# Kernel optimization log

Hardware: AMD Instinct MI355X
Metric: run time of the kernel (lower is better)

Reference implementation:

```python
import jax, jax.numpy as jnp
import numpy as np

B, L, D = 2, 2048, 1024
H = 16
HD = D // H  # 64


def setup_inputs() -> dict:
    key = jax.random.key(0)
    ks = jax.random.split(key, 7)
    s = 0.02
    return {
        "x": jax.random.normal(ks[0], (B, L, D), dtype=jnp.float32),
        "Wq": jax.random.normal(ks[1], (D, D), dtype=jnp.float32) * s,
        "bq": jnp.zeros((D,), dtype=jnp.float32),
        "Wkv": jax.random.normal(ks[2], (D, 2 * D), dtype=jnp.float32) * s,
        "bkv": jnp.zeros((2 * D,), dtype=jnp.float32),
        "Wo": jax.random.normal(ks[3], (D, D), dtype=jnp.float32) * s,
        "bo": jnp.zeros((D,), dtype=jnp.float32),
    }


def reference(x, Wq, bq, Wkv, bkv, Wo, bo):
    # q/kv projections (self-attention: key/value come from x)
    q = x @ Wq + bq                      # [B, L, D]
    kv = x @ Wkv + bkv                   # [B, L, 2D]
    k, v = jnp.split(kv, 2, axis=-1)     # each [B, L, D]
    # split heads: 'b l (h c) -> b h l c' (rope_embed_fraction=0 -> RoPE is identity)
    def heads(t):
        return t.reshape(B, L, H, HD).transpose(0, 2, 1, 3)
    qh, kh, vh = heads(q), heads(k), heads(v)   # [B, H, L, HD]
    scale = 1.0 / jnp.sqrt(jnp.asarray(HD, dtype=x.dtype))
    scores = jnp.einsum('bhqc,bhkc->bhqk', qh, kh) * scale  # [B, H, L, L]
    attn = jax.nn.softmax(scores, axis=-1)
    y = jnp.einsum('bhqk,bhkc->bhqc', attn, vh)             # [B, H, L, HD]
    # merge heads: 'b h l c -> b l (h c)'
    y = y.transpose(0, 2, 1, 3).reshape(B, L, D)
    return (y @ Wo + bo).reshape(x.shape)
```

## Files before the change

### kernel.cpp

```cpp
#include <hip/hip_runtime.h>

#define B_  2
#define L_  2048
#define D_  1024
#define H_  16
#define HD_ 64

typedef __attribute__((ext_vector_type(8))) short bf16x8;
typedef __attribute__((ext_vector_type(4))) float f32x4;

#define MFMA16(a, b, c) __builtin_amdgcn_mfma_f32_16x16x32_bf16(a, b, c, 0, 0, 0)

__device__ __forceinline__ unsigned short f2bf(float f) {
    union { float f; unsigned u; } v; v.f = f;
    unsigned r = v.u + 0x7FFFu + ((v.u >> 16) & 1u);
    return (unsigned short)(r >> 16);
}

__global__ __launch_bounds__(256) void prep_all(
    const float* __restrict__ x,
    const float* __restrict__ Wq, const float* __restrict__ Wkv,
    const float* __restrict__ Wo,
    unsigned short* __restrict__ xb,
    unsigned short* __restrict__ Wqt, unsigned short* __restrict__ Wkvt,
    unsigned short* __restrict__ Wot)
{
    const int z = blockIdx.z;
    if (z == 4) {
        const int bidl = blockIdx.y * 32 + blockIdx.x;
        const int n4 = B_ * L_ * D_ / 4;
        for (int i = bidl * 256 + threadIdx.x; i < n4; i += 1024 * 256) {
            float4 v = *(const float4*)(x + (size_t)i * 4);
            ushort4 u;
            u.x = f2bf(v.x); u.y = f2bf(v.y); u.z = f2bf(v.z); u.w = f2bf(v.w);
            *(ushort4*)(xb + (size_t)i * 4) = u;
        }
        return;
    }
    __shared__ float t[32][33];
    const float* W;  unsigned short* Wt;  int N, nc;
    if (z == 0)      { W = Wq;  Wt = Wqt;  N = 1024; nc = 0; }
    else if (z == 1) { W = Wo;  Wt = Wot;  N = 1024; nc = 0; }
    else             { W = Wkv; Wt = Wkvt; N = 2048; nc = (z - 2) * 1024; }
    const int tx = threadIdx.x & 31, ty = threadIdx.x >> 5;
    const int n0 = nc + blockIdx.x * 32, k0 = blockIdx.y * 32;
    #pragma unroll
    for (int r = 0; r < 4; ++r)
        t[ty + r * 8][tx] = W[(size_t)(k0 + ty + r * 8) * N + n0 + tx];
    __syncthreads();
    #pragma unroll
    for (int r = 0; r < 4; ++r)
        Wt[(size_t)(n0 + ty + r * 8) * 1024 + k0 + tx] = f2bf(t[tx][ty + r * 8]);
}

__global__ __launch_bounds__(512, 1) void gemm_qkv8(
    const unsigned short* __restrict__ A,
    const unsigned short* __restrict__ Bt,
    const float* __restrict__ bq, const float* __restrict__ bkv,
    unsigned short* __restrict__ Qb, unsigned short* __restrict__ Kb,
    unsigned short* __restrict__ Vtg, float qscl)
{
    const int KDIM = 1024, NT = 16;
    __shared__ __align__(16) unsigned short lds[65536];

    const int tid = threadIdx.x;
    const int w = tid >> 6, l = tid & 63, g = l >> 4, ln = l & 15;
    const int wm = (w >> 2) & 1, wn = w & 3;

    const int lin = blockIdx.x;
    const int wg = (lin & 7) * 24 + (lin >> 3);
    const int by = wg / 12, bx = wg % 12;
    const int m0 = by * 256, n0 = bx * 256;

    const int sr8 = w * 8 + (l >> 3);
    const int sc  = (l & 7) ^ ((l >> 3) & 7);
    const unsigned short* Asrc = A  + (size_t)m0 * KDIM + sc * 8;
    const unsigned short* Bsrc = Bt + (size_t)n0 * KDIM + sc * 8;

#define SLOT_A(d, h) (lds + ((d) * 2 + (h)) * 8192)
#define SLOT_B(d, h) (lds + 32768 + ((d) * 2 + (h)) * 8192)

#define STG(slotp, srcp, hh, kt_) do {                                        \
    _Pragma("unroll")                                                         \
    for (int r_ = 0; r_ < 2; ++r_) {                                          \
        const int row_ = (hh) * 128 + r_ * 64 + sr8;                          \
        __builtin_amdgcn_global_load_lds(                                     \
            (const __attribute__((address_space(1))) void*)                   \
                ((srcp) + (size_t)row_ * KDIM + (kt_) * 64),                  \
            (__attribute__((address_space(3))) void*)                         \
                ((slotp) + r_ * 4096 + w * 512 + l * 8),                      \
            16, 0, 0);                                                        \
    }                                                                         \
} while (0)

    f32x4 acc[8][4];
    #pragma unroll
    for (int i = 0; i < 8; ++i)
        #pragma unroll
        for (int j = 0; j < 4; ++j) acc[i][j] = (f32x4){0.f, 0.f, 0.f, 0.f};

    bf16x8 aR[4][2], bB0[2][2], bB1[2][2];

    STG(SLOT_A(0, 0), Asrc, 0, 0);
    STG(SLOT_B(0, 1), Bsrc, 1, 0);
    STG(SLOT_A(0, 1), Asrc, 1, 0);
    STG(SLOT_B(0, 0), Bsrc, 0, 0);
    STG(SLOT_A(1, 0), Asrc, 0, 1);
    STG(SLOT_B(1, 1), Bsrc, 1, 1);

    #pragma unroll 1
    for (int kt = 0; kt < NT; ++kt) {
        const int cur = kt & 1, nxt = cur ^ 1;
        asm volatile("s_waitcnt vmcnt(4)" ::: "memory");
        __builtin_amdgcn_s_barrier();

        #pragma unroll
        for (int mi = 0; mi < 4; ++mi)
            #pragma unroll
            for (int kc = 0; kc < 2; ++kc) {
                const int rho = wm * 64 + mi * 16 + ln, c = kc * 4 + g;
                aR[mi][kc] = *(const bf16x8*)
                    (SLOT_A(cur, 0) + rho * 64 + ((c ^ (rho & 7)) * 8));
            }
        #pragma unroll
        for (int ni = 0; ni < 2; ++ni)
            #pragma unroll
            for (int kc = 0; kc < 2; ++kc) {
                const int rho = wn * 32 + ni * 16 + ln, c = kc * 4 + g;
                bB0[ni][kc] = *(const bf16x8*)
                    (SLOT_B(cur, 0) + rho * 64 + ((c ^ (rho & 7)) * 8));
            }
        if (kt + 1 < NT) STG(SLOT_A(nxt, 1), Asrc, 1, kt + 1);
        __builtin_amdgcn_s_barrier();
        asm volatile("s_waitcnt lgkmcnt(0)" ::: "memory");
        __builtin_amdgcn_s_setprio(1);
        #pragma unroll
        for (int mi = 0; mi < 4; ++mi)
            #pragma unroll
            for (int ni = 0; ni < 2; ++ni) {
                acc[mi][ni] = MFMA16(aR[mi][0], bB0[ni][0], acc[mi][ni]);
                acc[mi][ni] = MFMA16(aR[mi][1], bB0[ni][1], acc[mi][ni]);
            }
        __builtin_amdgcn_s_setprio(0);
        __builtin_amdgcn_s_barrier();

        #pragma unroll
        for (int ni = 0; ni < 2; ++ni)
            #pragma unroll
            for (int kc = 0; kc < 2; ++kc) {
                const int rho = wn * 32 + ni * 16 + ln, c = kc * 4 + g;
                bB1[ni][kc] = *(const bf16x8*)
                    (SLOT_B(cur, 1) + rho * 64 + ((c ^ (rho & 7)) * 8));
            }
        if (kt + 1 < NT) STG(SLOT_B(nxt, 0), Bsrc, 0, kt + 1);
        __builtin_amdgcn_s_barrier();
        asm volatile("s_waitcnt lgkmcnt(0)" ::: "memory");
        __builtin_amdgcn_s_setprio(1);
        #pragma unroll
        for (int mi = 0; mi < 4; ++mi)
            #pragma unroll
            for (int ni = 0; ni < 2; ++ni) {
                acc[mi][2 + ni] = MFMA16(aR[mi][0], bB1[ni][0], acc[mi][2 + ni]);
                acc[mi][2 + ni] = MFMA16(aR[mi][1], bB1[ni][1], acc[mi][2 + ni]);
            }
        __builtin_amdgcn_s_setprio(0);
        __builtin_amdgcn_s_barrier();

        #pragma unroll
        for (int mi = 0; mi < 4; ++mi)
            #pragma unroll
            for (int kc = 0; kc < 2; ++kc) {
                const int rho = wm * 64 + mi * 16 + ln, c = kc * 4 + g;
                aR[mi][kc] = *(const bf16x8*)
                    (SLOT_A(cur, 1) + rho * 64 + ((c ^ (rho & 7)) * 8));
            }
        if (kt + 2 < NT) STG(SLOT_A(cur, 0), Asrc, 0, kt + 2);
        __builtin_amdgcn_s_barrier();
        asm volatile("s_waitcnt lgkmcnt(0)" ::: "memory");
        __builtin_amdgcn_s_setprio(1);
        #pragma unroll
        for (int mi = 0; mi < 4; ++mi)
            #pragma unroll
            for (int ni = 0; ni < 2; ++ni) {
                acc[4 + mi][2 + ni] = MFMA16(aR[mi][0], bB1[ni][0], acc[4 + mi][2 + ni]);
                acc[4 + mi][2 + ni] = MFMA16(aR[mi][1], bB1[ni][1], acc[4 + mi][2 + ni]);
            }
        __builtin_amdgcn_s_setprio(0);
        __builtin_amdgcn_s_barrier();

        if (kt + 2 < NT) STG(SLOT_B(cur, 1), Bsrc, 1, kt + 2);
        __builtin_amdgcn_s_barrier();
        __builtin_amdgcn_s_setprio(1);
        #pragma unroll
        for (int mi = 0; mi < 4; ++mi)
            #pragma unroll
            for (int ni = 0; ni < 2; ++ni) {
                acc[4 + mi][ni] = MFMA16(aR[mi][0], bB0[ni][0], acc[4 + mi][ni]);
                acc[4 + mi][ni] = MFMA16(aR[mi][1], bB0[ni][1], acc[4 + mi][ni]);
            }
        __builtin_amdgcn_s_setprio(0);
        __builtin_amdgcn_s_barrier();
    }
#undef STG
#undef SLOT_A
#undef SLOT_B

    const int region = n0 >> 10;
    if (region == 2) {
        #pragma unroll
        for (int nh = 0; nh < 2; ++nh)
            #pragma unroll
            for (int ni = 0; ni < 2; ++ni) {
                const int d = n0 - 2048 + nh * 128 + wn * 32 + ni * 16 + ln;
                const float bv = bkv[1024 + d];
                #pragma unroll
                for (int mh = 0; mh < 2; ++mh)
                    #pragma unroll
                    for (int mi = 0; mi < 4; ++mi) {
                        const int tok = m0 + mh * 128 + wm * 64 + mi * 16 + g * 4;
                        const int bb = tok >> 11, t4 = tok & 2047;
                        const f32x4 av = acc[mh * 4 + mi][nh * 2 + ni];
                        ushort4 p4;
                        p4.x = f2bf(av[0] + bv); p4.y = f2bf(av[1] + bv);
                        p4.z = f2bf(av[2] + bv); p4.w = f2bf(av[3] + bv);
                        *(ushort4*)(Vtg + ((size_t)bb * 1024 + d) * 2048 + t4) = p4;
                    }
            }
    } else {
        const int isQ = (region == 0);
        const float osc = isQ ? qscl : 1.f;
        #pragma unroll
        for (int nh = 0; nh < 2; ++nh)
            #pragma unroll
            for (int ni = 0; ni < 2; ++ni) {
                const int col = n0 + nh * 128 + wn * 32 + ni * 16 + ln;
                const float bv = isQ ? bq[col] : bkv[col - 1024];
                const int ck = isQ ? col : col - 1024;
                #pragma unroll
                for (int mh = 0; mh < 2; ++mh)
                    #pragma unroll
                    for (int mi = 0; mi < 4; ++mi) {
                        const int row = m0 + mh * 128 + wm * 64 + mi * 16 + g * 4;
                        const f32x4 av = acc[mh * 4 + mi][nh * 2 + ni];
                        #pragma unroll
                        for (int r = 0; r < 4; ++r) {
                            const float vout = (av[r] + bv) * osc;
                            if (isQ)
                                Qb[(size_t)(row + r) * 1024 + ck] = f2bf(vout);
                            else
                                Kb[(size_t)(row + r) * 1024 + ck] = f2bf(vout);
                        }
                    }
            }
    }
}

__global__ __launch_bounds__(256) void gemm_bt2(
    const unsigned short* __restrict__ A,
    const unsigned short* __restrict__ Bt,
    const float* __restrict__ bias,
    float* __restrict__ Cout)
{
    const int N = 1024, K = 1024;
    __shared__ __align__(16) unsigned short As[128 * 64];
    __shared__ __align__(16) unsigned short Bs[64 * 64];
    const int tid = threadIdx.x;
    const int w = tid >> 6, l = tid & 63, g = l >> 4, ln = l & 15;
    const int wm = w >> 1, wn = w & 1;
    const int dd = blockIdx.x;
    const int bid = (dd & 7) * 64 + (dd >> 3);
    const int m0 = (bid >> 4) * 128, n0 = (bid & 15) * 64;

    const int sr8 = w * 8 + (l >> 3);
    const int sc  = (l & 7) ^ ((l >> 3) & 7);
    const unsigned short* Asrc = A  + (size_t)m0 * K + sc * 8;
    const unsigned short* Bsrc = Bt + (size_t)n0 * K + sc * 8;

    f32x4 acc[4][2];
    #pragma unroll
    for (int i = 0; i < 4; ++i)
        #pragma unroll
        for (int j = 0; j < 2; ++j) acc[i][j] = (f32x4){0.f, 0.f, 0.f, 0.f};

    for (int k0 = 0; k0 < K; k0 += 64) {
        #pragma unroll
        for (int r_ = 0; r_ < 4; ++r_)
            __builtin_amdgcn_global_load_lds(
                (const __attribute__((address_space(1))) void*)
                    (Asrc + (size_t)(r_ * 32 + sr8) * K + k0),
                (__attribute__((address_space(3))) void*)
                    (As + r_ * 2048 + w * 512 + l * 8),
                16, 0, 0);
        #pragma unroll
        for (int r_ = 0; r_ < 2; ++r_)
            __builtin_amdgcn_global_load_lds(
                (const __attribute__((address_space(1))) void*)
                    (Bsrc + (size_t)(r_ * 32 + sr8) * K + k0),
                (__attribute__((address_space(3))) void*)
                    (Bs + r_ * 2048 + w * 512 + l * 8),
                16, 0, 0);
        __syncthreads();
        bf16x8 af[4][2], bfr[2][2];
        #pragma unroll
        for (int mi = 0; mi < 4; ++mi)
            #pragma unroll
            for (int kc = 0; kc < 2; ++kc) {
                const int rho = wm * 64 + mi * 16 + ln, c = kc * 4 + g;
                af[mi][kc] = *(const bf16x8*)
                    (As + rho * 64 + ((c ^ (rho & 7)) * 8));
            }
        #pragma unroll
        for (int ni = 0; ni < 2; ++ni)
            #pragma unroll
            for (int kc = 0; kc < 2; ++kc) {
                const int rho = wn * 32 + ni * 16 + ln, c = kc * 4 + g;
                bfr[ni][kc] = *(const bf16x8*)
                    (Bs + rho * 64 + ((c ^ (rho & 7)) * 8));
            }
        __builtin_amdgcn_s_setprio(1);
        #pragma unroll
        for (int mi = 0; mi < 4; ++mi)
            #pragma unroll
            for (int ni = 0; ni < 2; ++ni) {
                acc[mi][ni] = MFMA16(af[mi][0], bfr[ni][0], acc[mi][ni]);
                acc[mi][ni] = MFMA16(af[mi][1], bfr[ni][1], acc[mi][ni]);
            }
        __builtin_amdgcn_s_setprio(0);
        __syncthreads();
    }

    #pragma unroll
    for (int n = 0; n < 2; ++n) {
        const int col = n0 + wn * 32 + n * 16 + ln;
        const float bv = bias[col];
        #pragma unroll
        for (int m = 0; m < 4; ++m) {
            const int row = m0 + wm * 64 + m * 16 + g * 4;
            #pragma unroll
            for (int r = 0; r < 4; ++r)
                Cout[(size_t)(row + r) * N + col] = acc[m][n][r] + bv;
        }
    }
}

__global__ __launch_bounds__(256, 2) void attn_mfma(
    const unsigned short* __restrict__ Qb,
    const unsigned short* __restrict__ Kb,
    const unsigned short* __restrict__ Vtg,
    unsigned short* __restrict__ Yb)
{
    __shared__ __align__(16) unsigned short Ks[2][64 * 64];
    __shared__ __align__(16) unsigned short Vs[2][64 * 64];
    __shared__ __align__(16) unsigned short Pl[4][2][32 * 64];

    const int tid = threadIdx.x;
    const int w = tid >> 6, l = tid & 63, g = l >> 4, ln = l & 15;
    const int dd = blockIdx.x;
    const int bid = (dd & 7) * 64 + (dd >> 3);
    const int qc = bid & 15, h = (bid >> 4) & 15, b = bid >> 8;
    const int qrow = b * L_ + qc * 128 + w * 32;

    const int sub = l >> 3;
    const int scc = (l & 7) ^ sub;
    const unsigned short* ksrc = Kb  + (size_t)(b * L_) * 1024 + h * HD_ + scc * 8;
    const unsigned short* vsrc = Vtg + (size_t)(b * D_ + h * HD_) * 2048 + scc * 8;

#define STAGE(jj, bb) do {                                                    \
    _Pragma("unroll")                                                         \
    for (int i_ = 0; i_ < 2; ++i_) {                                          \
        const int rowK = w * 16 + i_ * 8 + sub;                               \
        __builtin_amdgcn_global_load_lds(                                     \
            (const __attribute__((address_space(1))) void*)                   \
                (ksrc + (size_t)((jj) * 64 + rowK) * 1024),                   \
            (__attribute__((address_space(3))) void*)                         \
                (&Ks[bb][w * 1024 + i_ * 512]), 16, 0, 0);                    \
        __builtin_amdgcn_global_load_lds(                                     \
            (const __attribute__((address_space(1))) void*)                   \
                (vsrc + (size_t)rowK * 2048 + (jj) * 64),                     \
            (__attribute__((address_space(3))) void*)                         \
                (&Vs[bb][w * 1024 + i_ * 512]), 16, 0, 0);                    \
    }                                                                         \
} while (0)

    bf16x8 qa[2][2];
    #pragma unroll
    for (int qt = 0; qt < 2; ++qt)
        #pragma unroll
        for (int c = 0; c < 2; ++c)
            qa[qt][c] = *(const bf16x8*)
                (Qb + (size_t)(qrow + qt * 16 + ln) * D_ + h * HD_ + c * 32 + g * 8);

    f32x4 o[2][4], lacc[2];
    #pragma unroll
    for (int qt = 0; qt < 2; ++qt) {
        #pragma unroll
        for (int dt = 0; dt < 4; ++dt) o[qt][dt] = (f32x4){0.f, 0.f, 0.f, 0.f};
        lacc[qt] = (f32x4){0.f, 0.f, 0.f, 0.f};
    }
    const short one_s = (short)0x3F80;
    const bf16x8 ones = {one_s, one_s, one_s, one_s, one_s, one_s, one_s, one_s};

    unsigned short* Pw = &Pl[w][0][0];
    const int swzl = (ln & 7) << 3;
    const int swp  = (ln & 7) << 1;

    bf16x8 vbA[4][2], vbB[4][2];

#define S_CORE(BUF, PWS, VARR) do {                                           \
    const unsigned short* Kc = &Ks[BUF][0];                                   \
    const unsigned short* Vc = &Vs[BUF][0];                                   \
    bf16x8 kb[4][2];                                                          \
    _Pragma("unroll")                                                         \
    for (int kt = 0; kt < 4; ++kt)                                            \
        _Pragma("unroll")                                                     \
        for (int c = 0; c < 2; ++c)                                           \
            kb[kt][c] = *(const bf16x8*)                                      \
                (Kc + (kt * 16 + ln) * 64 + ((c * 32 + g * 8) ^ swzl));       \
    f32x4 s[2][4];                                                            \
    const f32x4 z = (f32x4){0.f, 0.f, 0.f, 0.f};                              \
    __builtin_amdgcn_s_setprio(1);                                            \
    _Pragma("unroll")                                                         \
    for (int qt = 0; qt < 2; ++qt)                                            \
        _Pragma("unroll")                                                     \
        for (int kt = 0; kt < 4; ++kt) {                                      \
            f32x4 t0 = MFMA16(kb[kt][0], qa[qt][0], z);                       \
            s[qt][kt] = MFMA16(kb[kt][1], qa[qt][1], t0);                     \
        }                                                                     \
    __builtin_amdgcn_s_setprio(0);                                            \
    _Pragma("unroll")                                                         \
    for (int dt = 0; dt < 4; ++dt)                                            \
        _Pragma("unroll")                                                     \
        for (int c2 = 0; c2 < 2; ++c2)                                        \
            VARR[dt][c2] = *(const bf16x8*)                                   \
                (Vc + (dt * 16 + ln) * 64 + ((c2 * 32 + g * 8) ^ swzl));      \
    _Pragma("unroll")                                                         \
    for (int qt = 0; qt < 2; ++qt) {                                          \
        const int prow = (qt * 16 + ln) * 64;                                 \
        _Pragma("unroll")                                                     \
        for (int kt = 0; kt < 4; ++kt) {                                      \
            union { float f; unsigned u; } c0, c1, c2u, c3;                   \
            c0.f = __builtin_exp2f(s[qt][kt][0]);                             \
            c1.f = __builtin_exp2f(s[qt][kt][1]);                             \
            c2u.f = __builtin_exp2f(s[qt][kt][2]);                            \
            c3.f = __builtin_exp2f(s[qt][kt][3]);                             \
            uint2 pk;                                                         \
            pk.x = __builtin_amdgcn_perm(c1.u, c0.u, 0x07060302u);            \
            pk.y = __builtin_amdgcn_perm(c3.u, c2u.u, 0x07060302u);           \
            *(uint2*)(Pw + (PWS) * 2048 + prow +                              \
                      (((kt * 4 + g) ^ swp) << 2)) = pk;                      \
        }                                                                     \
    }                                                                         \
} while (0)

#define O_PHASE(PPWS, PVARR) do {                                             \
    bf16x8 pa[2][2];                                                          \
    _Pragma("unroll")                                                         \
    for (int qt = 0; qt < 2; ++qt)                                            \
        _Pragma("unroll")                                                     \
        for (int c2 = 0; c2 < 2; ++c2)                                        \
            pa[qt][c2] = *(const bf16x8*)                                     \
                (Pw + (PPWS) * 2048 + (qt * 16 + ln) * 64 +                   \
                 (((c2 * 8 + g * 2) ^ swp) << 2));                            \
    __builtin_amdgcn_s_setprio(1);                                            \
    _Pragma("unroll")                                                         \
    for (int qt = 0; qt < 2; ++qt) {                                          \
        lacc[qt] = MFMA16(pa[qt][0], ones, lacc[qt]);                         \
        lacc[qt] = MFMA16(pa[qt][1], ones, lacc[qt]);                         \
        _Pragma("unroll")                                                     \
        for (int dt = 0; dt < 4; ++dt) {                                      \
            o[qt][dt] = MFMA16(pa[qt][0], PVARR[dt][0], o[qt][dt]);           \
            o[qt][dt] = MFMA16(pa[qt][1], PVARR[dt][1], o[qt][dt]);           \
        }                                                                     \
    }                                                                         \
    __builtin_amdgcn_s_setprio(0);                                            \
} while (0)

    STAGE(0, 0);
    __syncthreads();

    STAGE(1, 1);
    S_CORE(0, 0, vbA);
    __syncthreads();

    #pragma unroll 1
    for (int t = 1; t < 31; t += 2) {
        STAGE(t + 1, 0);
        O_PHASE(0, vbA);
        S_CORE(1, 1, vbB);
        __syncthreads();
        if (t + 2 < 32) STAGE(t + 2, 1);
        O_PHASE(1, vbB);
        S_CORE(0, 0, vbA);
        __syncthreads();
    }

    O_PHASE(0, vbA);
    S_CORE(1, 1, vbB);
    O_PHASE(1, vbB);
#undef O_PHASE
#undef S_CORE
#undef STAGE

    #pragma unroll
    for (int qt = 0; qt < 2; ++qt)
        #pragma unroll
        for (int r = 0; r < 4; ++r) {
            const float inv = 1.f / lacc[qt][r];
            const int row = qrow + qt * 16 + g * 4 + r;
            #pragma unroll
            for (int dt = 0; dt < 4; ++dt)
                Yb[(size_t)row * D_ + h * HD_ + dt * 16 + ln] =
                    f2bf(o[qt][dt][r] * inv);
        }
}

extern "C" void kernel_launch(void* const* d_in, const int* in_sizes, int n_in,
                              void* d_out, int out_size, void* d_ws, size_t ws_size,
                              hipStream_t stream)
{
    const float* x   = (const float*)d_in[0];
    const float* Wq  = (const float*)d_in[1];
    const float* bq  = (const float*)d_in[2];
    const float* Wkv = (const float*)d_in[3];
    const float* bkv = (const float*)d_in[4];
    const float* Wo  = (const float*)d_in[5];
    const float* bo  = (const float*)d_in[6];
    float* out = (float*)d_out;

    const int M = B_ * L_;
    unsigned short* ws = (unsigned short*)d_ws;
    unsigned short* xb   = ws;
    unsigned short* Wqt  = xb   + (size_t)M * D_;
    unsigned short* Wkvt = Wqt  + (size_t)D_ * D_;
    unsigned short* Wot  = Wkvt + (size_t)2 * D_ * D_;
    unsigned short* Qb   = Wot  + (size_t)D_ * D_;
    unsigned short* Kb   = Qb   + (size_t)M * D_;
    unsigned short* Vtg  = Kb   + (size_t)M * D_;
    unsigned short* Yb   = Vtg  + (size_t)B_ * D_ * L_;

    const float QSCL = 0.125f * 1.44269504089f;

    prep_all<<<dim3(32, 32, 5), 256, 0, stream>>>(
        x, Wq, Wkv, Wo, xb, Wqt, Wkvt, Wot);

    gemm_qkv8<<<dim3(192), 512, 0, stream>>>(xb, Wqt, bq, bkv, Qb, Kb, Vtg, QSCL);

    attn_mfma<<<dim3(B_ * H_ * (L_ / 128)), 256, 0, stream>>>(Qb, Kb, Vtg, Yb);

    gemm_bt2<<<dim3(512), 256, 0, stream>>>(Yb, Wot, bo, out);
}
```

Baseline: 123.7 us.

## Halve QKV GEMM N-tile to 128 and deepen K-step in output GEMM

The QKV projection GEMM tile shrinks from 256x256 to 256x128, doubling the grid from 192 to 384 workgroups so all CUs on the 256-CU part get work instead of leaving many idle. LDS use and the accumulator count drop accordingly. Separately, the output projection GEMM now stages 128 of K per iteration instead of 64, halving the number of barrier pairs per tile at the cost of more LDS and registers. Smaller QKV tiles lower arithmetic intensity and add redundant A-tile traffic.

```diff
diff --git a/kernel.cpp b/kernel.cpp
--- a/kernel.cpp
+++ b/kernel.cpp
@@ -61,16 +61,16 @@
     unsigned short* __restrict__ Vtg, float qscl)
 {
     const int KDIM = 1024, NT = 16;
-    __shared__ __align__(16) unsigned short lds[65536];
+    __shared__ __align__(16) unsigned short lds[49152];
 
     const int tid = threadIdx.x;
     const int w = tid >> 6, l = tid & 63, g = l >> 4, ln = l & 15;
     const int wm = (w >> 2) & 1, wn = w & 3;
 
     const int lin = blockIdx.x;
-    const int wg = (lin & 7) * 24 + (lin >> 3);
-    const int by = wg / 12, bx = wg % 12;
-    const int m0 = by * 256, n0 = bx * 256;
+    const int wg = (lin & 7) * 48 + (lin >> 3);
+    const int by = wg / 24, bx = wg % 24;
+    const int m0 = by * 256, n0 = bx * 128;
 
     const int sr8 = w * 8 + (l >> 3);
     const int sc  = (l & 7) ^ ((l >> 3) & 7);
@@ -78,40 +78,50 @@
     const unsigned short* Bsrc = Bt + (size_t)n0 * KDIM + sc * 8;
 
 #define SLOT_A(d, h) (lds + ((d) * 2 + (h)) * 8192)
-#define SLOT_B(d, h) (lds + 32768 + ((d) * 2 + (h)) * 8192)
-
-#define STG(slotp, srcp, hh, kt_) do {                                        \
+#define SLOT_B(d, h) (lds + 32768 + ((d) * 2 + (h)) * 4096)
+
+#define STGA(slotp, hh, kt_) do {                                             \
     _Pragma("unroll")                                                         \
     for (int r_ = 0; r_ < 2; ++r_) {                                          \
         const int row_ = (hh) * 128 + r_ * 64 + sr8;                          \
         __builtin_amdgcn_global_load_lds(                                     \
             (const __attribute__((address_space(1))) void*)                   \
-                ((srcp) + (size_t)row_ * KDIM + (kt_) * 64),                  \
+                (Asrc + (size_t)row_ * KDIM + (kt_) * 64),                    \
             (__attribute__((address_space(3))) void*)                         \
                 ((slotp) + r_ * 4096 + w * 512 + l * 8),                      \
             16, 0, 0);                                                        \
     }                                                                         \
 } while (0)
 
-    f32x4 acc[8][4];
+#define STGB(slotp, hh, kt_) do {                                             \
+    const int row_ = (hh) * 64 + sr8;                                         \
+    __builtin_amdgcn_global_load_lds(                                         \
+        (const __attribute__((address_space(1))) void*)                       \
+            (Bsrc + (size_t)row_ * KDIM + (kt_) * 64),                        \
+        (__attribute__((address_space(3))) void*)                             \
+            ((slotp) + w * 512 + l * 8),                                      \
+        16, 0, 0);                                                            \
+} while (0)
+
+    f32x4 acc[8][2];
     #pragma unroll
     for (int i = 0; i < 8; ++i)
         #pragma unroll
-        for (int j = 0; j < 4; ++j) acc[i][j] = (f32x4){0.f, 0.f, 0.f, 0.f};
-
-    bf16x8 aR[4][2], bB0[2][2], bB1[2][2];
-
-    STG(SLOT_A(0, 0), Asrc, 0, 0);
-    STG(SLOT_B(0, 1), Bsrc, 1, 0);
-    STG(SLOT_A(0, 1), Asrc, 1, 0);
-    STG(SLOT_B(0, 0), Bsrc, 0, 0);
-    STG(SLOT_A(1, 0), Asrc, 0, 1);
-    STG(SLOT_B(1, 1), Bsrc, 1, 1);
+        for (int j = 0; j < 2; ++j) acc[i][j] = (f32x4){0.f, 0.f, 0.f, 0.f};
+
+    bf16x8 aR[4][2], bB0[2], bB1[2];
+
+    STGA(SLOT_A(0, 0), 0, 0);
+    STGB(SLOT_B(0, 1), 1, 0);
+    STGA(SLOT_A(0, 1), 1, 0);
+    STGB(SLOT_B(0, 0), 0, 0);
+    STGA(SLOT_A(1, 0), 0, 1);
+    STGB(SLOT_B(1, 1), 1, 1);
 
     #pragma unroll 1
     for (int kt = 0; kt < NT; ++kt) {
         const int cur = kt & 1, nxt = cur ^ 1;
-        asm volatile("s_waitcnt vmcnt(4)" ::: "memory");
+        asm volatile("s_waitcnt vmcnt(3)" ::: "memory");
         __builtin_amdgcn_s_barrier();
 
         #pragma unroll
@@ -123,46 +133,38 @@
                     (SLOT_A(cur, 0) + rho * 64 + ((c ^ (rho & 7)) * 8));
             }
         #pragma unroll
-        for (int ni = 0; ni < 2; ++ni)
-            #pragma unroll
-            for (int kc = 0; kc < 2; ++kc) {
-                const int rho = wn * 32 + ni * 16 + ln, c = kc * 4 + g;
-                bB0[ni][kc] = *(const bf16x8*)
-                    (SLOT_B(cur, 0) + rho * 64 + ((c ^ (rho & 7)) * 8));
-            }
-        if (kt + 1 < NT) STG(SLOT_A(nxt, 1), Asrc, 1, kt + 1);
+        for (int kc = 0; kc < 2; ++kc) {
+            const int rho = wn * 16 + ln, c = kc * 4 + g;
+            bB0[kc] = *(const bf16x8*)
+                (SLOT_B(cur, 0) + rho * 64 + ((c ^ (rho & 7)) * 8));
+        }
+        if (kt + 1 < NT) STGA(SLOT_A(nxt, 1), 1, kt + 1);
         __builtin_amdgcn_s_barrier();
         asm volatile("s_waitcnt lgkmcnt(0)" ::: "memory");
         __builtin_amdgcn_s_setprio(1);
         #pragma unroll
-        for (int mi = 0; mi < 4; ++mi)
-            #pragma unroll
-            for (int ni = 0; ni < 2; ++ni) {
-                acc[mi][ni] = MFMA16(aR[mi][0], bB0[ni][0], acc[mi][ni]);
-                acc[mi][ni] = MFMA16(aR[mi][1], bB0[ni][1], acc[mi][ni]);
-            }
+        for (int mi = 0; mi < 4; ++mi) {
+            acc[mi][0] = MFMA16(aR[mi][0], bB0[0], acc[mi][0]);
+            acc[mi][0] = MFMA16(aR[mi][1], bB0[1], acc[mi][0]);
+        }
         __builtin_amdgcn_s_setprio(0);
         __builtin_amdgcn_s_barrier();
 
         #pragma unroll
-        for (int ni = 0; ni < 2; ++ni)
-            #pragma unroll
-            for (int kc = 0; kc < 2; ++kc) {
-                const int rho = wn * 32 + ni * 16 + ln, c = kc * 4 + g;
-                bB1[ni][kc] = *(const bf16x8*)
-                    (SLOT_B(cur, 1) + rho * 64 + ((c ^ (rho & 7)) * 8));
-            }
-        if (kt + 1 < NT) STG(SLOT_B(nxt, 0), Bsrc, 0, kt + 1);
+        for (int kc = 0; kc < 2; ++kc) {
+            const int rho = wn * 16 + ln, c = kc * 4 + g;
+            bB1[kc] = *(const bf16x8*)
+                (SLOT_B(cur, 1) + rho * 64 + ((c ^ (rho & 7)) * 8));
+        }
+        if (kt + 1 < NT) STGB(SLOT_B(nxt, 0), 0, kt + 1);
         __builtin_amdgcn_s_barrier();
         asm volatile("s_waitcnt lgkmcnt(0)" ::: "memory");
         __builtin_amdgcn_s_setprio(1);
         #pragma unroll
-        for (int mi = 0; mi < 4; ++mi)
-            #pragma unroll
-            for (int ni = 0; ni < 2; ++ni) {
-                acc[mi][2 + ni] = MFMA16(aR[mi][0], bB1[ni][0], acc[mi][2 + ni]);
-                acc[mi][2 + ni] = MFMA16(aR[mi][1], bB1[ni][1], acc[mi][2 + ni]);
-            }
+        for (int mi = 0; mi < 4; ++mi) {
+            acc[mi][1] = MFMA16(aR[mi][0], bB1[0], acc[mi][1]);
+            acc[mi][1] = MFMA16(aR[mi][1], bB1[1], acc[mi][1]);
+        }
         __builtin_amdgcn_s_setprio(0);
         __builtin_amdgcn_s_barrier();
 
@@ -174,84 +176,77 @@
                 aR[mi][kc] = *(const bf16x8*)
                     (SLOT_A(cur, 1) + rho * 64 + ((c ^ (rho & 7)) * 8));
             }
-        if (kt + 2 < NT) STG(SLOT_A(cur, 0), Asrc, 0, kt + 2);
+        if (kt + 2 < NT) STGA(SLOT_A(cur, 0), 0, kt + 2);
         __builtin_amdgcn_s_barrier();
         asm volatile("s_waitcnt lgkmcnt(0)" ::: "memory");
         __builtin_amdgcn_s_setprio(1);
         #pragma unroll
-        for (int mi = 0; mi < 4; ++mi)
-            #pragma unroll
-            for (int ni = 0; ni < 2; ++ni) {
-                acc[4 + mi][2 + ni] = MFMA16(aR[mi][0], bB1[ni][0], acc[4 + mi][2 + ni]);
-                acc[4 + mi][2 + ni] = MFMA16(aR[mi][1], bB1[ni][1], acc[4 + mi][2 + ni]);
-            }
+        for (int mi = 0; mi < 4; ++mi) {
+            acc[4 + mi][1] = MFMA16(aR[mi][0], bB1[0], acc[4 + mi][1]);
+            acc[4 + mi][1] = MFMA16(aR[mi][1], bB1[1], acc[4 + mi][1]);
+        }
         __builtin_amdgcn_s_setprio(0);
         __builtin_amdgcn_s_barrier();
 
-        if (kt + 2 < NT) STG(SLOT_B(cur, 1), Bsrc, 1, kt + 2);
+        if (kt + 2 < NT) STGB(SLOT_B(cur, 1), 1, kt + 2);
         __builtin_amdgcn_s_barrier();
         __builtin_amdgcn_s_setprio(1);
         #pragma unroll
-        for (int mi = 0; mi < 4; ++mi)
-            #pragma unroll
-            for (int ni = 0; ni < 2; ++ni) {
-                acc[4 + mi][ni] = MFMA16(aR[mi][0], bB0[ni][0], acc[4 + mi][ni]);
-                acc[4 + mi][ni] = MFMA16(aR[mi][1], bB0[ni][1], acc[4 + mi][ni]);
-            }
+        for (int mi = 0; mi < 4; ++mi) {
+            acc[4 + mi][0] = MFMA16(aR[mi][0], bB0[0], acc[4 + mi][0]);
+            acc[4 + mi][0] = MFMA16(aR[mi][1], bB0[1], acc[4 + mi][0]);
+        }
         __builtin_amdgcn_s_setprio(0);
         __builtin_amdgcn_s_barrier();
     }
-#undef STG
+#undef STGA
+#undef STGB
 #undef SLOT_A
 #undef SLOT_B
 
     const int region = n0 >> 10;
     if (region == 2) {
         #pragma unroll
-        for (int nh = 0; nh < 2; ++nh)
-            #pragma unroll
-            for (int ni = 0; ni < 2; ++ni) {
-                const int d = n0 - 2048 + nh * 128 + wn * 32 + ni * 16 + ln;
-                const float bv = bkv[1024 + d];
+        for (int nh = 0; nh < 2; ++nh) {
+            const int d = n0 - 2048 + nh * 64 + wn * 16 + ln;
+            const float bv = bkv[1024 + d];
+            #pragma unroll
+            for (int mh = 0; mh < 2; ++mh)
                 #pragma unroll
-                for (int mh = 0; mh < 2; ++mh)
-                    #pragma unroll
-                    for (int mi = 0; mi < 4; ++mi) {
-                        const int tok = m0 + mh * 128 + wm * 64 + mi * 16 + g * 4;
-                        const int bb = tok >> 11, t4 = tok & 2047;
-                        const f32x4 av = acc[mh * 4 + mi][nh * 2 + ni];
-                        ushort4 p4;
-                        p4.x = f2bf(av[0] + bv); p4.y = f2bf(av[1] + bv);
-                        p4.z = f2bf(av[2] + bv); p4.w = f2bf(av[3] + bv);
-                        *(ushort4*)(Vtg + ((size_t)bb * 1024 + d) * 2048 + t4) = p4;
-                    }
-            }
+                for (int mi = 0; mi < 4; ++mi) {
+                    const int tok = m0 + mh * 128 + wm * 64 + mi * 16 + g * 4;
+                    const int bb = tok >> 11, t4 = tok & 2047;
+                    const f32x4 av = acc[mh * 4 + mi][nh];
+                    ushort4 p4;
+                    p4.x = f2bf(av[0] + bv); p4.y = f2bf(av[1] + bv);
+                    p4.z = f2bf(av[2] + bv); p4.w = f2bf(av[3] + bv);
+                    *(ushort4*)(Vtg + ((size_t)bb * 1024 + d) * 2048 + t4) = p4;
+                }
+        }
     } else {
         const int isQ = (region == 0);
         const float osc = isQ ? qscl : 1.f;
         #pragma unroll
-        for (int nh = 0; nh < 2; ++nh)
-            #pragma unroll
-            for (int ni = 0; ni < 2; ++ni) {
-                const int col = n0 + nh * 128 + wn * 32 + ni * 16 + ln;
-                const float bv = isQ ? bq[col] : bkv[col - 1024];
-                const int ck = isQ ? col : col - 1024;
+        for (int nh = 0; nh < 2; ++nh) {
+            const int col = n0 + nh * 64 + wn * 16 + ln;
+            const float bv = isQ ? bq[col] : bkv[col - 1024];
+            const int ck = isQ ? col : col - 1024;
+            #pragma unroll
+            for (int mh = 0; mh < 2; ++mh)
                 #pragma unroll
-                for (int mh = 0; mh < 2; ++mh)
+                for (int mi = 0; mi < 4; ++mi) {
+                    const int row = m0 + mh * 128 + wm * 64 + mi * 16 + g * 4;
+                    const f32x4 av = acc[mh * 4 + mi][nh];
                     #pragma unroll
-                    for (int mi = 0; mi < 4; ++mi) {
-                        const int row = m0 + mh * 128 + wm * 64 + mi * 16 + g * 4;
-                        const f32x4 av = acc[mh * 4 + mi][nh * 2 + ni];
-                        #pragma unroll
-                        for (int r = 0; r < 4; ++r) {
-                            const float vout = (av[r] + bv) * osc;
-                            if (isQ)
-                                Qb[(size_t)(row + r) * 1024 + ck] = f2bf(vout);
-                            else
-                                Kb[(size_t)(row + r) * 1024 + ck] = f2bf(vout);
-                        }
+                    for (int r = 0; r < 4; ++r) {
+                        const float vout = (av[r] + bv) * osc;
+                        if (isQ)
+                            Qb[(size_t)(row + r) * 1024 + ck] = f2bf(vout);
+                        else
+                            Kb[(size_t)(row + r) * 1024 + ck] = f2bf(vout);
                     }
-            }
+                }
+        }
     }
 }
 
@@ -262,8 +257,8 @@
     float* __restrict__ Cout)
 {
     const int N = 1024, K = 1024;
-    __shared__ __align__(16) unsigned short As[128 * 64];
-    __shared__ __align__(16) unsigned short Bs[64 * 64];
+    __shared__ __align__(16) unsigned short As[2 * 128 * 64];
+    __shared__ __align__(16) unsigned short Bs[2 * 64 * 64];
     const int tid = threadIdx.x;
     const int w = tid >> 6, l = tid & 63, g = l >> 4, ln = l & 15;
     const int wm = w >> 1, wn = w & 1;
@@ -282,49 +277,52 @@
         #pragma unroll
         for (int j = 0; j < 2; ++j) acc[i][j] = (f32x4){0.f, 0.f, 0.f, 0.f};
 
-    for (int k0 = 0; k0 < K; k0 += 64) {
-        #pragma unroll
-        for (int r_ = 0; r_ < 4; ++r_)
-            __builtin_amdgcn_global_load_lds(
-                (const __attribute__((address_space(1))) void*)
-                    (Asrc + (size_t)(r_ * 32 + sr8) * K + k0),
-                (__attribute__((address_space(3))) void*)
-                    (As + r_ * 2048 + w * 512 + l * 8),
-                16, 0, 0);
-        #pragma unroll
-        for (int r_ = 0; r_ < 2; ++r_)
-            __builtin_amdgcn_global_load_lds(
-                (const __attribute__((address_space(1))) void*)
-                    (Bsrc + (size_t)(r_ * 32 + sr8) * K + k0),
-                (__attribute__((address_space(3))) void*)
-                    (Bs + r_ * 2048 + w * 512 + l * 8),
-                16, 0, 0);
+    for (int k0 = 0; k0 < K; k0 += 128) {
+        #pragma unroll
+        for (int ks = 0; ks < 2; ++ks) {
+            #pragma unroll
+            for (int r_ = 0; r_ < 4; ++r_)
+                __builtin_amdgcn_global_load_lds(
+                    (const __attribute__((address_space(1))) void*)
+                        (Asrc + (size_t)(r_ * 32 + sr8) * K + k0 + ks * 64),
+                    (__attribute__((address_space(3))) void*)
+                        (As + ks * 8192 + r_ * 2048 + w * 512 + l * 8),
+                    16, 0, 0);
+            #pragma unroll
+            for (int r_ = 0; r_ < 2; ++r_)
+                __builtin_amdgcn_global_load_lds(
+                    (const __attribute__((address_space(1))) void*)
+                        (Bsrc + (size_t)(r_ * 32 + sr8) * K + k0 + ks * 64),
+                    (__attribute__((address_space(3))) void*)
+                        (Bs + ks * 4096 + r_ * 2048 + w * 512 + l * 8),
+                    16, 0, 0);
+        }
         __syncthreads();
-        bf16x8 af[4][2], bfr[2][2];
+        bf16x8 af[4][4], bfr[2][4];
         #pragma unroll
         for (int mi = 0; mi < 4; ++mi)
             #pragma unroll
-            for (int kc = 0; kc < 2; ++kc) {
+            for (int kc = 0; kc < 4; ++kc) {
                 const int rho = wm * 64 + mi * 16 + ln, c = kc * 4 + g;
                 af[mi][kc] = *(const bf16x8*)
-                    (As + rho * 64 + ((c ^ (rho & 7)) * 8));
+                    (As + (c >> 3) * 8192 + rho * 64 + (((c & 7) ^ (rho & 7)) * 8));
             }
         #pragma unroll
         for (int ni = 0; ni < 2; ++ni)
             #pragma unroll
-            for (int kc = 0; kc < 2; ++kc) {
+            for (int kc = 0; kc < 4; ++kc) {
                 const int rho = wn * 32 + ni * 16 + ln, c = kc * 4 + g;
                 bfr[ni][kc] = *(const bf16x8*)
-                    (Bs + rho * 64 + ((c ^ (rho & 7)) * 8));
+                    (Bs + (c >> 3) * 4096 + rho * 64 + (((c & 7) ^ (rho & 7)) * 8));
             }
         __builtin_amdgcn_s_setprio(1);
         #pragma unroll
         for (int mi = 0; mi < 4; ++mi)
             #pragma unroll
-            for (int ni = 0; ni < 2; ++ni) {
-                acc[mi][ni] = MFMA16(af[mi][0], bfr[ni][0], acc[mi][ni]);
-                acc[mi][ni] = MFMA16(af[mi][1], bfr[ni][1], acc[mi][ni]);
-            }
+            for (int ni = 0; ni < 2; ++ni)
+                #pragma unroll
+                for (int kc = 0; kc < 4; ++kc)
+                    acc[mi][ni] = MFMA16(af[mi][kc], bfr[ni][kc], acc[mi][ni]);
         __builtin_amdgcn_s_setprio(0);
         __syncthreads();
     }
@@ -543,7 +541,7 @@
     prep_all<<<dim3(32, 32, 5), 256, 0, stream>>>(
         x, Wq, Wkv, Wo, xb, Wqt, Wkvt, Wot);
 
-    gemm_qkv8<<<dim3(192), 512, 0, stream>>>(xb, Wqt, bq, bkv, Qb, Kb, Vtg, QSCL);
+    gemm_qkv8<<<dim3(384), 512, 0, stream>>>(xb, Wqt, bq, bkv, Qb, Kb, Vtg, QSCL);
 
     attn_mfma<<<dim3(B_ * H_ * (L_ / 128)), 256, 0, stream>>>(Qb, Kb, Vtg, Yb);
 
```

Result: slower. 127.5 us (+3.1%).

## Retile QKV GEMM to 128x384 blocks to fill all 256 CUs

Applied to the files above, without the earlier changes.

Changes the QKV projection GEMM tile from 256x256 (192 blocks) to 128x384 (256 blocks), so the grid matches the 256 compute units instead of leaving about a quarter idle. The LDS slots, staging macros, per-wave fragment shapes and epilogue are reworked for the new tile, and the epilogue now picks the Q/K/V region per column because a 384-wide tile can straddle region boundaries. Tail-iteration prefetches are clamped to redundant loads rather than skipped, which keeps the vmcnt accounting uniform. In exchange, each tile does less arithmetic per byte loaded, so more global and LDS traffic per FLOP.

```diff
diff --git a/kernel.cpp b/kernel.cpp
--- a/kernel.cpp
+++ b/kernel.cpp
@@ -68,76 +68,87 @@
     const int wm = (w >> 2) & 1, wn = w & 3;
 
     const int lin = blockIdx.x;
-    const int wg = (lin & 7) * 24 + (lin >> 3);
-    const int by = wg / 12, bx = wg % 12;
-    const int m0 = by * 256, n0 = bx * 256;
+    const int wg = (lin & 7) * 32 + (lin >> 3);
+    const int by = wg >> 3, bx = wg & 7;
+    const int m0 = by * 128, n0 = bx * 384;
 
     const int sr8 = w * 8 + (l >> 3);
     const int sc  = (l & 7) ^ ((l >> 3) & 7);
     const unsigned short* Asrc = A  + (size_t)m0 * KDIM + sc * 8;
     const unsigned short* Bsrc = Bt + (size_t)n0 * KDIM + sc * 8;
 
-#define SLOT_A(d, h) (lds + ((d) * 2 + (h)) * 8192)
-#define SLOT_B(d, h) (lds + 32768 + ((d) * 2 + (h)) * 8192)
-
-#define STG(slotp, srcp, hh, kt_) do {                                        \
-    _Pragma("unroll")                                                         \
-    for (int r_ = 0; r_ < 2; ++r_) {                                          \
-        const int row_ = (hh) * 128 + r_ * 64 + sr8;                          \
+#define SLOT_A(d, h) (lds + ((d) * 2 + (h)) * 4096)
+#define SLOT_B(d, h) (lds + 16384 + ((d) * 2 + (h)) * 12288)
+
+#define STGA(slotp, hh, kt_) do {                                             \
+    const int rowA_ = (hh) * 64 + sr8;                                        \
+    __builtin_amdgcn_global_load_lds(                                         \
+        (const __attribute__((address_space(1))) void*)                       \
+            (Asrc + (size_t)rowA_ * KDIM + (kt_) * 64),                       \
+        (__attribute__((address_space(3))) void*)((slotp) + tid * 8),         \
+        16, 0, 0);                                                            \
+} while (0)
+
+#define STGB(slotp, hh, kt_) do {                                             \
+    _Pragma("unroll")                                                         \
+    for (int r_ = 0; r_ < 3; ++r_) {                                          \
+        const int rowB_ = (hh) * 192 + r_ * 64 + sr8;                         \
         __builtin_amdgcn_global_load_lds(                                     \
             (const __attribute__((address_space(1))) void*)                   \
-                ((srcp) + (size_t)row_ * KDIM + (kt_) * 64),                  \
+                (Bsrc + (size_t)rowB_ * KDIM + (kt_) * 64),                   \
             (__attribute__((address_space(3))) void*)                         \
-                ((slotp) + r_ * 4096 + w * 512 + l * 8),                      \
+                ((slotp) + r_ * 4096 + tid * 8),                              \
             16, 0, 0);                                                        \
     }                                                                         \
 } while (0)
 
-    f32x4 acc[8][4];
-    #pragma unroll
-    for (int i = 0; i < 8; ++i)
-        #pragma unroll
-        for (int j = 0; j < 4; ++j) acc[i][j] = (f32x4){0.f, 0.f, 0.f, 0.f};
-
-    bf16x8 aR[4][2], bB0[2][2], bB1[2][2];
-
-    STG(SLOT_A(0, 0), Asrc, 0, 0);
-    STG(SLOT_B(0, 1), Bsrc, 1, 0);
-    STG(SLOT_A(0, 1), Asrc, 1, 0);
-    STG(SLOT_B(0, 0), Bsrc, 0, 0);
-    STG(SLOT_A(1, 0), Asrc, 0, 1);
-    STG(SLOT_B(1, 1), Bsrc, 1, 1);
+    f32x4 acc[4][6];
+    #pragma unroll
+    for (int i = 0; i < 4; ++i)
+        #pragma unroll
+        for (int j = 0; j < 6; ++j) acc[i][j] = (f32x4){0.f, 0.f, 0.f, 0.f};
+
+    bf16x8 aR[2][2], bB0[3][2], bB1[3][2];
+
+    STGA(SLOT_A(0, 0), 0, 0);
+    STGB(SLOT_B(0, 1), 1, 0);
+    STGA(SLOT_A(0, 1), 1, 0);
+    STGB(SLOT_B(0, 0), 0, 0);
+    STGA(SLOT_A(1, 0), 0, 1);
+    STGB(SLOT_B(1, 1), 1, 1);
 
     #pragma unroll 1
     for (int kt = 0; kt < NT; ++kt) {
         const int cur = kt & 1, nxt = cur ^ 1;
+        const int kt1 = (kt + 1 < NT) ? kt + 1 : NT - 1;
+        const int kt2 = (kt + 2 < NT) ? kt + 2 : NT - 1;
         asm volatile("s_waitcnt vmcnt(4)" ::: "memory");
         __builtin_amdgcn_s_barrier();
 
         #pragma unroll
-        for (int mi = 0; mi < 4; ++mi)
+        for (int mi = 0; mi < 2; ++mi)
             #pragma unroll
             for (int kc = 0; kc < 2; ++kc) {
-                const int rho = wm * 64 + mi * 16 + ln, c = kc * 4 + g;
+                const int rho = wm * 32 + mi * 16 + ln, c = kc * 4 + g;
                 aR[mi][kc] = *(const bf16x8*)
                     (SLOT_A(cur, 0) + rho * 64 + ((c ^ (rho & 7)) * 8));
             }
         #pragma unroll
-        for (int ni = 0; ni < 2; ++ni)
+        for (int ni = 0; ni < 3; ++ni)
             #pragma unroll
             for (int kc = 0; kc < 2; ++kc) {
-                const int rho = wn * 32 + ni * 16 + ln, c = kc * 4 + g;
+                const int rho = wn * 48 + ni * 16 + ln, c = kc * 4 + g;
                 bB0[ni][kc] = *(const bf16x8*)
                     (SLOT_B(cur, 0) + rho * 64 + ((c ^ (rho & 7)) * 8));
             }
-        if (kt + 1 < NT) STG(SLOT_A(nxt, 1), Asrc, 1, kt + 1);
+        STGA(SLOT_A(nxt, 1), 1, kt1);
         __builtin_amdgcn_s_barrier();
         asm volatile("s_waitcnt lgkmcnt(0)" ::: "memory");
         __builtin_amdgcn_s_setprio(1);
         #pragma unroll
-        for (int mi = 0; mi < 4; ++mi)
-            #pragma unroll
-            for (int ni = 0; ni < 2; ++ni) {
+        for (int mi = 0; mi < 2; ++mi)
+            #pragma unroll
+            for (int ni = 0; ni < 3; ++ni) {
                 acc[mi][ni] = MFMA16(aR[mi][0], bB0[ni][0], acc[mi][ni]);
                 acc[mi][ni] = MFMA16(aR[mi][1], bB0[ni][1], acc[mi][ni]);
             }
@@ -145,103 +156,99 @@
         __builtin_amdgcn_s_barrier();
 
         #pragma unroll
-        for (int ni = 0; ni < 2; ++ni)
+        for (int ni = 0; ni < 3; ++ni)
             #pragma unroll
             for (int kc = 0; kc < 2; ++kc) {
-                const int rho = wn * 32 + ni * 16 + ln, c = kc * 4 + g;
+                const int rho = wn * 48 + ni * 16 + ln, c = kc * 4 + g;
                 bB1[ni][kc] = *(const bf16x8*)
                     (SLOT_B(cur, 1) + rho * 64 + ((c ^ (rho & 7)) * 8));
             }
-        if (kt + 1 < NT) STG(SLOT_B(nxt, 0), Bsrc, 0, kt + 1);
+        STGB(SLOT_B(nxt, 0), 0, kt1);
         __builtin_amdgcn_s_barrier();
         asm volatile("s_waitcnt lgkmcnt(0)" ::: "memory");
         __builtin_amdgcn_s_setprio(1);
         #pragma unroll
-        for (int mi = 0; mi < 4; ++mi)
-            #pragma unroll
-            for (int ni = 0; ni < 2; ++ni) {
-                acc[mi][2 + ni] = MFMA16(aR[mi][0], bB1[ni][0], acc[mi][2 + ni]);
-                acc[mi][2 + ni] = MFMA16(aR[mi][1], bB1[ni][1], acc[mi][2 + ni]);
+        for (int mi = 0; mi < 2; ++mi)
+            #pragma unroll
+            for (int ni = 0; ni < 3; ++ni) {
+                acc[mi][3 + ni] = MFMA16(aR[mi][0], bB1[ni][0], acc[mi][3 + ni]);
+                acc[mi][3 + ni] = MFMA16(aR[mi][1], bB1[ni][1], acc[mi][3 + ni]);
             }
         __builtin_amdgcn_s_setprio(0);
         __builtin_amdgcn_s_barrier();
 
         #pragma unroll
-        for (int mi = 0; mi < 4; ++mi)
+        for (int mi = 0; mi < 2; ++mi)
             #pragma unroll
             for (int kc = 0; kc < 2; ++kc) {
-                const int rho = wm * 64 + mi * 16 + ln, c = kc * 4 + g;
+                const int rho = wm * 32 + mi * 16 + ln, c = kc * 4 + g;
                 aR[mi][kc] = *(const bf16x8*)
                     (SLOT_A(cur, 1) + rho * 64 + ((c ^ (rho & 7)) * 8));
             }
-        if (kt + 2 < NT) STG(SLOT_A(cur, 0), Asrc, 0, kt + 2);
+        STGA(SLOT_A(cur, 0), 0, kt2);
         __builtin_amdgcn_s_barrier();
         asm volatile("s_waitcnt lgkmcnt(0)" ::: "memory");
         __builtin_amdgcn_s_setprio(1);
         #pragma unroll
-        for (int mi = 0; mi < 4; ++mi)
-            #pragma unroll
-            for (int ni = 0; ni < 2; ++ni) {
-                acc[4 + mi][2 + ni] = MFMA16(aR[mi][0], bB1[ni][0], acc[4 + mi][2 + ni]);
-                acc[4 + mi][2 + ni] = MFMA16(aR[mi][1], bB1[ni][1], acc[4 + mi][2 + ni]);
+        for (int mi = 0; mi < 2; ++mi)
+            #pragma unroll
+            for (int ni = 0; ni < 3; ++ni) {
+                acc[2 + mi][3 + ni] = MFMA16(aR[mi][0], bB1[ni][0], acc[2 + mi][3 + ni]);
+                acc[2 + mi][3 + ni] = MFMA16(aR[mi][1], bB1[ni][1], acc[2 + mi][3 + ni]);
             }
         __builtin_amdgcn_s_setprio(0);
         __builtin_amdgcn_s_barrier();
 
-        if (kt + 2 < NT) STG(SLOT_B(cur, 1), Bsrc, 1, kt + 2);
+        STGB(SLOT_B(cur, 1), 1, kt2);
         __builtin_amdgcn_s_barrier();
         __builtin_amdgcn_s_setprio(1);
         #pragma unroll
-        for (int mi = 0; mi < 4; ++mi)
-            #pragma unroll
-            for (int ni = 0; ni < 2; ++ni) {
-                acc[4 + mi][ni] = MFMA16(aR[mi][0], bB0[ni][0], acc[4 + mi][ni]);
-                acc[4 + mi][ni] = MFMA16(aR[mi][1], bB0[ni][1], acc[4 + mi][ni]);
+        for (int mi = 0; mi < 2; ++mi)
+            #pragma unroll
+            for (int ni = 0; ni < 3; ++ni) {
+                acc[2 + mi][ni] = MFMA16(aR[mi][0], bB0[ni][0], acc[2 + mi][ni]);
+                acc[2 + mi][ni] = MFMA16(aR[mi][1], bB0[ni][1], acc[2 + mi][ni]);
             }
         __builtin_amdgcn_s_setprio(0);
         __builtin_amdgcn_s_barrier();
     }
-#undef STG
+#undef STGA
+#undef STGB
 #undef SLOT_A
 #undef SLOT_B
 
-    const int region = n0 >> 10;
-    if (region == 2) {
-        #pragma unroll
-        for (int nh = 0; nh < 2; ++nh)
-            #pragma unroll
-            for (int ni = 0; ni < 2; ++ni) {
-                const int d = n0 - 2048 + nh * 128 + wn * 32 + ni * 16 + ln;
+    #pragma unroll
+    for (int nh = 0; nh < 2; ++nh)
+        #pragma unroll
+        for (int ni = 0; ni < 3; ++ni) {
+            const int col = n0 + nh * 192 + wn * 48 + ni * 16 + ln;
+            const int region = col >> 10;
+            if (region == 2) {
+                const int d = col - 2048;
                 const float bv = bkv[1024 + d];
                 #pragma unroll
                 for (int mh = 0; mh < 2; ++mh)
                     #pragma unroll
-                    for (int mi = 0; mi < 4; ++mi) {
-                        const int tok = m0 + mh * 128 + wm * 64 + mi * 16 + g * 4;
+                    for (int mi = 0; mi < 2; ++mi) {
+                        const int tok = m0 + mh * 64 + wm * 32 + mi * 16 + g * 4;
                         const int bb = tok >> 11, t4 = tok & 2047;
-                        const f32x4 av = acc[mh * 4 + mi][nh * 2 + ni];
+                        const f32x4 av = acc[mh * 2 + mi][nh * 3 + ni];
                         ushort4 p4;
                         p4.x = f2bf(av[0] + bv); p4.y = f2bf(av[1] + bv);
                         p4.z = f2bf(av[2] + bv); p4.w = f2bf(av[3] + bv);
                         *(ushort4*)(Vtg + ((size_t)bb * 1024 + d) * 2048 + t4) = p4;
                     }
-            }
-    } else {
-        const int isQ = (region == 0);
-        const float osc = isQ ? qscl : 1.f;
-        #pragma unroll
-        for (int nh = 0; nh < 2; ++nh)
-            #pragma unroll
-            for (int ni = 0; ni < 2; ++ni) {
-                const int col = n0 + nh * 128 + wn * 32 + ni * 16 + ln;
+            } else {
+                const int isQ = (region == 0);
+                const float osc = isQ ? qscl : 1.f;
                 const float bv = isQ ? bq[col] : bkv[col - 1024];
                 const int ck = isQ ? col : col - 1024;
                 #pragma unroll
                 for (int mh = 0; mh < 2; ++mh)
                     #pragma unroll
-                    for (int mi = 0; mi < 4; ++mi) {
-                        const int row = m0 + mh * 128 + wm * 64 + mi * 16 + g * 4;
-                        const f32x4 av = acc[mh * 4 + mi][nh * 2 + ni];
+                    for (int mi = 0; mi < 2; ++mi) {
+                        const int row = m0 + mh * 64 + wm * 32 + mi * 16 + g * 4;
+                        const f32x4 av = acc[mh * 2 + mi][nh * 3 + ni];
                         #pragma unroll
                         for (int r = 0; r < 4; ++r) {
                             const float vout = (av[r] + bv) * osc;
@@ -252,7 +259,7 @@
                         }
                     }
             }
-    }
+        }
 }
 
 __global__ __launch_bounds__(256) void gemm_bt2(
@@ -543,7 +550,7 @@
     prep_all<<<dim3(32, 32, 5), 256, 0, stream>>>(
         x, Wq, Wkv, Wo, xb, Wqt, Wkvt, Wot);
 
-    gemm_qkv8<<<dim3(192), 512, 0, stream>>>(xb, Wqt, bq, bkv, Qb, Kb, Vtg, QSCL);
+    gemm_qkv8<<<dim3(256), 512, 0, stream>>>(xb, Wqt, bq, bkv, Qb, Kb, Vtg, QSCL);
 
     attn_mfma<<<dim3(B_ * H_ * (L_ / 128)), 256, 0, stream>>>(Qb, Kb, Vtg, Yb);
 
```

Measured after the change: 119.6 us. 3.3% less time.
